# Kernel optimization log

Measured on AMD Instinct MI355X. Metric: run time of the kernel, lower is better.

## Reference

```python
import jax, jax.numpy as jnp
import numpy as np

H = 8          # n_heads
D_MODEL = 512
D_HEAD = 64    # d_keys = d_values = d_model // n_heads


def _fft_feats(x):
    # x: (B, L, C) real -> (B, C, L_fft, 3) stacking [real, imag, rfftfreq]
    n = x.shape[1]
    xf = jnp.fft.rfft(jnp.swapaxes(x, 1, 2), axis=-1)  # (B, C, L_fft) complex
    freqs = jnp.fft.rfftfreq(n).astype(x.dtype)        # (L_fft,)
    f = jnp.broadcast_to(freqs, xf.shape)
    return jnp.stack([xf.real.astype(x.dtype), xf.imag.astype(x.dtype), f], axis=-1)


def _proj_heads(feats, W, b):
    # Conv1d(kernel=3, stride=3) over the flattened (L_fft*3) axis is exactly a
    # per-frequency contraction over the 3 stacked features.
    # feats: (B, C, F, 3), W: (O, C, 3), b: (O,) -> (B, F, H, O//H)
    y = jnp.einsum('bcfk,ock->bfo', feats, W) + b
    B, F, O = y.shape
    return y.reshape(B, F, H, O // H)


def setup_inputs() -> dict:
    key = jax.random.key(0)
    ks = jax.random.split(key, 8)
    B, L, S = 16, 2048, 2048
    q = jax.random.normal(ks[0], (B, L, D_MODEL), jnp.float32)
    k = jax.random.normal(ks[1], (B, S, D_MODEL), jnp.float32)
    v = jax.random.normal(ks[2], (B, S, D_MODEL), jnp.float32)
    O = H * D_HEAD
    s = 1.0 / np.sqrt(3.0 * D_MODEL)
    Wq = jax.random.normal(ks[3], (O, D_MODEL, 3), jnp.float32) * s
    Wk = jax.random.normal(ks[4], (O, D_MODEL, 3), jnp.float32) * s
    Wv = jax.random.normal(ks[5], (O, D_MODEL, 3), jnp.float32) * s
    bq = jnp.zeros((O,), jnp.float32)
    bk = jnp.zeros((O,), jnp.float32)
    bv = jnp.zeros((O,), jnp.float32)
    Wo = jax.random.normal(ks[6], (2 * D_MODEL, O), jnp.float32) * (1.0 / np.sqrt(O))
    bo = jnp.zeros((2 * D_MODEL,), jnp.float32)
    return {"queries": q, "keys": k, "values": v,
            "Wq": Wq, "bq": bq, "Wk": Wk, "bk": bk, "Wv": Wv, "bv": bv,
            "Wo": Wo, "bo": bo}


def reference(queries, keys, values, Wq, bq, Wk, bk, Wv, bv, Wo, bo):
    B, L, _ = queries.shape
    qh = _proj_heads(_fft_feats(queries), Wq, bq)  # (B, Lf, H, E)
    kh = _proj_heads(_fft_feats(keys), Wk, bk)     # (B, Sf, H, E)
    vh = _proj_heads(_fft_feats(values), Wv, bv)   # (B, Sf, H, D)
    scale = 1.0 / jnp.sqrt(jnp.asarray(qh.shape[-1], qh.dtype))
    scores = jnp.einsum('blhe,bshe->bhls', qh, kh)
    attn = jax.nn.softmax(scale * scores, axis=-1)  # (B, H, Lf, Sf)
    ctx = jnp.einsum('bhls,bshd->blhd', attn, vh)   # (B, Lf, H, D)
    Lf = ctx.shape[1]
    ctx = ctx.reshape(B, Lf, H * D_HEAD)
    y = ctx @ Wo.T + bo                              # (B, Lf, 2*d_model)
    y = y.reshape(B, Lf, D_MODEL, 2)
    yc = jax.lax.complex(y[..., 0], y[..., 1])       # (B, Lf, d_model)
    out = jnp.fft.irfft(jnp.swapaxes(yc, 1, 2), n=L, axis=-1)  # (B, d_model, L)
    return jnp.swapaxes(out, 1, 2), attn
```

## Files before the change

### kernel.cpp

```cpp
#include <hip/hip_runtime.h>
#include <math.h>

#define FL 1025

typedef __bf16 bf16x8 __attribute__((ext_vector_type(8)));
typedef float  f32x4  __attribute__((ext_vector_type(4)));

static __device__ __forceinline__ bf16x8 ldfrag(const __bf16* p) {
  union { uint4 q; bf16x8 v; } u;
  u.q = *(const uint4*)p;
  return u.v;
}
static __device__ __forceinline__ float fexp(float x) { return __expf(x); }

static __device__ __forceinline__ void fft2048_stages(float* re, float* im, int tid, int dir) {
  for (int len = 2; len <= 2048; len <<= 1) {
    int half = len >> 1;
    __syncthreads();
    for (int t = tid; t < 1024; t += 256) {
      int j  = t & (half - 1);
      int i0 = ((t & ~(half - 1)) << 1) | j;
      int i1 = i0 + half;
      float ang = (2.0f * (float)j) / (float)len;
      float wr = cospif(ang);
      float s  = sinpif(ang);
      float wi = (dir > 0) ? s : -s;
      float vr = re[i1], vi = im[i1];
      float tr = vr * wr - vi * wi;
      float ti = vr * wi + vi * wr;
      float ur = re[i0], ui = im[i0];
      re[i0] = ur + tr; im[i0] = ui + ti;
      re[i1] = ur - tr; im[i1] = ui - ti;
    }
  }
  __syncthreads();
}

__global__ __launch_bounds__(256) void rfft3_kernel(const float* __restrict__ xT,
                                                    float* __restrict__ QF3) {
  __shared__ float re[2048];
  __shared__ float im[2048];
  int c2 = blockIdx.x, b = blockIdx.y, t = blockIdx.z, tid = threadIdx.x;
  const float* pa = xT + (((long long)t * 16 + b) * 512 + 2 * c2) * 2048;
  const float* pb = pa + 2048;
  float4 a0 = *(const float4*)(pa + tid * 8);
  float4 a1 = *(const float4*)(pa + tid * 8 + 4);
  float4 b0 = *(const float4*)(pb + tid * 8);
  float4 b1 = *(const float4*)(pb + tid * 8 + 4);
  float va[8] = {a0.x, a0.y, a0.z, a0.w, a1.x, a1.y, a1.z, a1.w};
  float vb[8] = {b0.x, b0.y, b0.z, b0.w, b1.x, b1.y, b1.z, b1.w};
#pragma unroll
  for (int j = 0; j < 8; j++) {
    int l = tid * 8 + j;
    int r = __brev((unsigned)l) >> 21;
    re[r] = va[j];
    im[r] = vb[j];
  }
  fft2048_stages(re, im, tid, -1);
  float* base = QF3 + ((long long)t * 16 + b) * 1052672;
  for (int f = tid; f <= 1024; f += 256) {
    int g = (2048 - f) & 2047;
    float fr = re[f], fi = im[f], gr = re[g], gi = im[g];
    float Xar = 0.5f * (fr + gr), Xai = 0.5f * (fi - gi);
    float Xbr = 0.5f * (fi + gi), Xbi = 0.5f * (gr - fr);
    base[(long long)(2 * c2) * 1028 + f]       = Xar;
    base[(long long)(512 + 2 * c2) * 1028 + f] = Xai;
    base[(long long)(2 * c2 + 1) * 1028 + f]   = Xbr;
    base[(long long)(513 + 2 * c2) * 1028 + f] = Xbi;
  }
}

__global__ __launch_bounds__(256) void irfft3_kernel(const float* __restrict__ ybT,
                                                     float* __restrict__ out) {
  __shared__ float Yar[FL], Yai[FL], Ybr[FL], Ybi[FL];
  __shared__ float re[2048];
  __shared__ float im[2048];
  int d2 = blockIdx.x, b = blockIdx.y, tid = threadIdx.x;
  const float* yp = ybT + ((long long)b * 1024 + 4 * d2) * 1025;
  for (int f = tid; f <= 1024; f += 256) {
    Yar[f] = yp[f];
    Yai[f] = yp[1025 + f];
    Ybr[f] = yp[2050 + f];
    Ybi[f] = yp[3075 + f];
  }
  __syncthreads();
  if (tid == 0) { Yai[0] = 0.f; Yai[1024] = 0.f; Ybi[0] = 0.f; Ybi[1024] = 0.f; }
  __syncthreads();
  for (int i = tid; i < 2048; i += 256) {
    int j = __brev((unsigned)i) >> 21;
    float rr, ii;
    if (j <= 1024) { rr = Yar[j] - Ybi[j]; ii = Yai[j] + Ybr[j]; }
    else { int f = 2048 - j; rr = Yar[f] + Ybi[f]; ii = Ybr[f] - Yai[f]; }
    re[i] = rr; im[i] = ii;
  }
  fft2048_stages(re, im, tid, +1);
  float* op = out + (long long)b * 2048 * 512 + 2 * d2;
  const float sc = 1.0f / 2048.0f;
  for (int l = tid; l < 2048; l += 256) {
    float2 v = {re[l] * sc, im[l] * sc};
    *(float2*)(op + (long long)l * 512) = v;
  }
}

__global__ __launch_bounds__(256) void transpose_x(const float* __restrict__ q,
                                                   const float* __restrict__ k,
                                                   const float* __restrict__ v,
                                                   float* __restrict__ xT) {
  __shared__ float t[32][33];
  int z = blockIdx.z;
  int ti = z >> 4, b = z & 15;
  const float* x = (ti == 0) ? q : (ti == 1) ? k : v;
  int l0 = blockIdx.x * 32, c0 = blockIdx.y * 32;
  int tx = threadIdx.x & 31, ty = threadIdx.x >> 5;
  for (int i = ty; i < 32; i += 8)
    t[i][tx] = x[((long long)b * 2048 + l0 + i) * 512 + c0 + tx];
  __syncthreads();
  float* dst = xT + ((long long)ti * 16 + b) * 512 * 2048;
  for (int i = ty; i < 32; i += 8)
    dst[((long long)(c0 + i)) * 2048 + l0 + tx] = t[tx][i];
}

__global__ __launch_bounds__(256) void setup_pack(
    const float* __restrict__ Wq, const float* __restrict__ Wk,
    const float* __restrict__ Wv, const float* __restrict__ Wo,
    const float* __restrict__ bq, const float* __restrict__ bk,
    const float* __restrict__ bv,
    __bf16* __restrict__ Wth, __bf16* __restrict__ Wtl,
    __bf16* __restrict__ Woh, float* __restrict__ wf3, float* __restrict__ bias3) {
  int bx = blockIdx.x, tid = threadIdx.x;
  if (bx < 6144) {
    int e = bx * 256 + tid;
    int t = e >> 19, local = e & 524287;
    const float* W = (t == 0) ? Wq : (t == 1) ? Wk : Wv;
    int o = local >> 10, kk = local & 1023;
    int c = kk & 511, j = kk >> 9;
    float v = W[(long long)o * 1536 + c * 3 + j];
    __bf16 h = (__bf16)v;
    Wth[e] = h;
    Wtl[e] = (__bf16)(v - (float)h);
  } else if (bx < 8192) {
    int e = (bx - 6144) * 256 + tid;
    Woh[e] = (__bf16)Wo[e];
  } else if (bx < 8198) {
    int idx = (bx - 8192) * 256 + tid;
    int t = idx / 512, o = idx & 511;
    const float* W = (t == 0) ? Wq : (t == 1) ? Wk : Wv;
    float s = 0.f;
    for (int c = 0; c < 512; c++) s += W[(long long)o * 1536 + c * 3 + 2];
    wf3[idx] = s;
  } else {
    int idx = (bx - 8198) * 256 + tid;
    int t = idx / 512, o = idx & 511;
    bias3[idx] = (t == 0) ? bq[o] : (t == 1) ? bk[o] : bv[o];
  }
}

__global__ __launch_bounds__(256) void proj_gemm(
    const float* __restrict__ QF3,
    const __bf16* __restrict__ Wth, const __bf16* __restrict__ Wtl,
    const float* __restrict__ wf3, const float* __restrict__ bias3,
    __bf16* __restrict__ qhh, __bf16* __restrict__ qhl,
    __bf16* __restrict__ khh, __bf16* __restrict__ khl,
    __bf16* __restrict__ vhT, float uscale) {
  __shared__ __bf16 As[2][128][40];
  __shared__ __bf16 Bs[2][128][40];
  int tid = threadIdx.x;
  int wid = tid >> 6, lane = tid & 63;
  int lrow = lane & 15, quad = lane >> 4;
  int m0 = blockIdx.x * 128, n0 = blockIdx.y * 128;
  int z = blockIdx.z;
  int t = z >> 4, b = z & 15;
  const float* Ab = QF3 + (long long)z * 1052672;
  const __bf16* Bbh = Wth + (long long)t * 524288;
  const __bf16* Bbl = Wtl + (long long)t * 524288;

  int wm0 = (wid & 1) * 64, wn0 = (wid >> 1) * 64;
  int floc = tid & 127;
  int kg = (tid >> 7) * 4;
  const float* Acol = Ab + min(m0 + floc, 1024);
  int srow = tid >> 1, shalf = tid & 1;

  f32x4 acc[4][4];
#pragma unroll
  for (int i = 0; i < 4; i++)
#pragma unroll
    for (int j = 0; j < 4; j++) acc[i][j] = (f32x4){0.f, 0.f, 0.f, 0.f};

  for (int k0 = 0; k0 < 1024; k0 += 32) {
#pragma unroll
    for (int it = 0; it < 4; it++) {
      int kko = kg + it * 8;
      float v0 = Acol[(long long)(k0 + kko + 0) * 1028];
      float v1 = Acol[(long long)(k0 + kko + 1) * 1028];
      float v2 = Acol[(long long)(k0 + kko + 2) * 1028];
      float v3 = Acol[(long long)(k0 + kko + 3) * 1028];
      __bf16 h0 = (__bf16)v0, h1 = (__bf16)v1, h2 = (__bf16)v2, h3 = (__bf16)v3;
      unsigned short u0, u1, u2, u3;
      __builtin_memcpy(&u0, &h0, 2); __builtin_memcpy(&u1, &h1, 2);
      __builtin_memcpy(&u2, &h2, 2); __builtin_memcpy(&u3, &h3, 2);
      uint2 hu = make_uint2((unsigned)u0 | ((unsigned)u1 << 16),
                            (unsigned)u2 | ((unsigned)u3 << 16));
      __bf16 l0 = (__bf16)(v0 - (float)h0), l1 = (__bf16)(v1 - (float)h1);
      __bf16 l2 = (__bf16)(v2 - (float)h2), l3 = (__bf16)(v3 - (float)h3);
      __builtin_memcpy(&u0, &l0, 2); __builtin_memcpy(&u1, &l1, 2);
      __builtin_memcpy(&u2, &l2, 2); __builtin_memcpy(&u3, &l3, 2);
      uint2 lu = make_uint2((unsigned)u0 | ((unsigned)u1 << 16),
                            (unsigned)u2 | ((unsigned)u3 << 16));
      *(uint2*)&As[0][floc][kko] = hu;
      *(uint2*)&As[1][floc][kko] = lu;
    }
    {
      const __bf16* s = Bbh + (long long)(n0 + srow) * 1024 + k0 + shalf * 16;
      uint4* d = (uint4*)&Bs[0][srow][shalf * 16];
      d[0] = ((const uint4*)s)[0]; d[1] = ((const uint4*)s)[1];
      s = Bbl + (long long)(n0 + srow) * 1024 + k0 + shalf * 16;
      d = (uint4*)&Bs[1][srow][shalf * 16];
      d[0] = ((const uint4*)s)[0]; d[1] = ((const uint4*)s)[1];
    }
    __syncthreads();

    bf16x8 bh[4], bl[4];
#pragma unroll
    for (int nt = 0; nt < 4; nt++) {
      int r = wn0 + nt * 16 + lrow;
      bh[nt] = ldfrag(&Bs[0][r][quad * 8]);
      bl[nt] = ldfrag(&Bs[1][r][quad * 8]);
    }
#pragma unroll
    for (int mt = 0; mt < 4; mt++) {
      int r = wm0 + mt * 16 + lrow;
      bf16x8 ah = ldfrag(&As[0][r][quad * 8]);
      bf16x8 al = ldfrag(&As[1][r][quad * 8]);
#pragma unroll
      for (int nt = 0; nt < 4; nt++) {
        acc[mt][nt] = __builtin_amdgcn_mfma_f32_16x16x32_bf16(ah, bh[nt], acc[mt][nt], 0, 0, 0);
        acc[mt][nt] = __builtin_amdgcn_mfma_f32_16x16x32_bf16(ah, bl[nt], acc[mt][nt], 0, 0, 0);
        acc[mt][nt] = __builtin_amdgcn_mfma_f32_16x16x32_bf16(al, bh[nt], acc[mt][nt], 0, 0, 0);
      }
    }
    __syncthreads();
  }

  __bf16* Ch = (t == 0) ? qhh : khh;
  __bf16* Cl = (t == 0) ? qhl : khl;
#pragma unroll
  for (int mt = 0; mt < 4; mt++) {
#pragma unroll
    for (int nt = 0; nt < 4; nt++) {
      int gn = n0 + wn0 + nt * 16 + lrow;
      float bn = bias3[t * 512 + gn];
      float vn = wf3[t * 512 + gn];
      int gmb = m0 + wm0 + mt * 16 + quad * 4;
      if (t < 2) {
#pragma unroll
        for (int r = 0; r < 4; r++) {
          int gm = gmb + r;
          if (gm < FL) {
            float val = acc[mt][nt][r] + bn + uscale * (float)gm * vn;
            long long o = ((long long)b * FL + gm) * 512 + gn;
            __bf16 h = (__bf16)val;
            Ch[o] = h;
            Cl[o] = (__bf16)(val - (float)h);
          }
        }
      } else {
        int hh = gn >> 6, dd = gn & 63;
        long long ob = ((long long)(b * 8 + hh) * 64 + dd) * 1152;
#pragma unroll
        for (int r = 0; r < 4; r++) {
          int gm = gmb + r;
          if (gm < FL) {
            float val = acc[mt][nt][r] + bn + uscale * (float)gm * vn;
            vhT[ob + gm] = (__bf16)val;
          }
        }
      }
    }
  }
}

__global__ __launch_bounds__(256) void oproj_gemm(
    const __bf16* __restrict__ ctx, const __bf16* __restrict__ Woh,
    const float* __restrict__ bo, float* __restrict__ ybT) {
  __shared__ __bf16 As[128][40];
  __shared__ __bf16 Bs[128][40];
  int tid = threadIdx.x;
  int wid = tid >> 6, lane = tid & 63;
  int lrow = lane & 15, quad = lane >> 4;
  int m0 = blockIdx.x * 128, n0 = blockIdx.y * 128;
  int z = blockIdx.z;
  const __bf16* Ab = ctx + (long long)z * 524800;
  int wm0 = (wid & 1) * 64, wn0 = (wid >> 1) * 64;
  int srow = tid >> 1, shalf = tid & 1;
  int arow = min(m0 + srow, FL - 1);

  f32x4 acc[4][4];
#pragma unroll
  for (int i = 0; i < 4; i++)
#pragma unroll
    for (int j = 0; j < 4; j++) acc[i][j] = (f32x4){0.f, 0.f, 0.f, 0.f};

  for (int k0 = 0; k0 < 512; k0 += 32) {
    {
      const __bf16* s = Ab + (long long)arow * 512 + k0 + shalf * 16;
      uint4* d = (uint4*)&As[srow][shalf * 16];
      d[0] = ((const uint4*)s)[0]; d[1] = ((const uint4*)s)[1];
      s = Woh + (long long)(n0 + srow) * 512 + k0 + shalf * 16;
      d = (uint4*)&Bs[srow][shalf * 16];
      d[0] = ((const uint4*)s)[0]; d[1] = ((const uint4*)s)[1];
    }
    __syncthreads();
    bf16x8 bh[4];
#pragma unroll
    for (int nt = 0; nt < 4; nt++) bh[nt] = ldfrag(&Bs[wn0 + nt * 16 + lrow][quad * 8]);
#pragma unroll
    for (int mt = 0; mt < 4; mt++) {
      bf16x8 ah = ldfrag(&As[wm0 + mt * 16 + lrow][quad * 8]);
#pragma unroll
      for (int nt = 0; nt < 4; nt++)
        acc[mt][nt] = __builtin_amdgcn_mfma_f32_16x16x32_bf16(ah, bh[nt], acc[mt][nt], 0, 0, 0);
    }
    __syncthreads();
  }

#pragma unroll
  for (int mt = 0; mt < 4; mt++) {
#pragma unroll
    for (int nt = 0; nt < 4; nt++) {
      int gn = n0 + wn0 + nt * 16 + lrow;
      float bn = bo[gn];
      int gmb = m0 + wm0 + mt * 16 + quad * 4;
      long long ob = (long long)z * 1049600 + (long long)gn * 1025;
#pragma unroll
      for (int r = 0; r < 4; r++) {
        int gm = gmb + r;
        if (gm < FL) ybT[ob + gm] = acc[mt][nt][r] + bn;
      }
    }
  }
}

static __device__ __forceinline__ void compute_S_tile(
    const __bf16 (*Kh)[72], const __bf16 (*Kl)[72],
    const bf16x8 (&qf)[2][2], int lrow, int quad, int n0, f32x4* sa) {
#pragma unroll
  for (int nt = 0; nt < 8; nt++) sa[nt] = (f32x4){0.f, 0.f, 0.f, 0.f};
#pragma unroll
  for (int kit = 0; kit < 2; kit++) {
#pragma unroll
    for (int nt = 0; nt < 8; nt++) {
      bf16x8 kh = ldfrag(&Kh[nt * 16 + lrow][kit * 32 + quad * 8]);
      bf16x8 kl = ldfrag(&Kl[nt * 16 + lrow][kit * 32 + quad * 8]);
      sa[nt] = __builtin_amdgcn_mfma_f32_16x16x32_bf16(qf[0][kit], kh, sa[nt], 0, 0, 0);
      sa[nt] = __builtin_amdgcn_mfma_f32_16x16x32_bf16(qf[0][kit], kl, sa[nt], 0, 0, 0);
      sa[nt] = __builtin_amdgcn_mfma_f32_16x16x32_bf16(qf[1][kit], kh, sa[nt], 0, 0, 0);
    }
  }
#pragma unroll
  for (int nt = 0; nt < 8; nt++) {
    int gn = n0 + nt * 16 + lrow;
    bool ok = gn < FL;
#pragma unroll
    for (int r = 0; r < 4; r++) sa[nt][r] = ok ? sa[nt][r] * 0.125f : -INFINITY;
  }
}

__global__ __launch_bounds__(512) void flash_kernel(
    const __bf16* __restrict__ qh_h, const __bf16* __restrict__ qh_l,
    const __bf16* __restrict__ kh_h, const __bf16* __restrict__ kh_l,
    const __bf16* __restrict__ vhT,
    float* __restrict__ attn, __bf16* __restrict__ ctxb) {
  __shared__ __align__(16) char smem[54272];
  __bf16 (*Kh)[72]  = (__bf16 (*)[72])smem;
  __bf16 (*Kl)[72]  = (__bf16 (*)[72])(smem + 18432);
  __bf16 (*P)[136]  = (__bf16 (*)[136])smem;
  __bf16 (*Bv)[136] = (__bf16 (*)[136])(smem + 36864);

  int tid = threadIdx.x;
  int wid = tid >> 6, lane = tid & 63;
  int lrow = lane & 15, quad = lane >> 4;
  int f0 = blockIdx.x * 128;
  int z = blockIdx.z;
  int b = z >> 3, h = z & 7;

  bf16x8 qf[2][2];
  {
    int rowq = min(f0 + wid * 16 + lrow, FL - 1);
    long long base = ((long long)b * FL + rowq) * 512 + h * 64 + quad * 8;
#pragma unroll
    for (int kit = 0; kit < 2; kit++) {
      qf[0][kit] = ldfrag(qh_h + base + kit * 32);
      qf[1][kit] = ldfrag(qh_l + base + kit * 32);
    }
  }

  int sp = tid >> 8, srw = (tid >> 1) & 127, shalf = tid & 1;
  const __bf16* ksrc0 = (sp ? kh_l : kh_h) + (long long)b * FL * 512 + h * 64 + shalf * 32;
  __bf16* kdst = (sp ? Kl[srw] : Kh[srw]) + shalf * 32;

  float m_i[4], l_i[4];
#pragma unroll
  for (int r = 0; r < 4; r++) { m_i[r] = -INFINITY; l_i[r] = 0.f; }

  f32x4 sa[8];

  for (int nt0 = 0; nt0 < 9; nt0++) {
    __syncthreads();
    {
      int srowg = min(nt0 * 128 + srw, FL - 1);
      const __bf16* s = ksrc0 + (long long)srowg * 512;
#pragma unroll
      for (int u = 0; u < 4; u++) ((uint4*)kdst)[u] = ((const uint4*)s)[u];
    }
    __syncthreads();
    compute_S_tile(Kh, Kl, qf, lrow, quad, nt0 * 128, sa);
#pragma unroll
    for (int r = 0; r < 4; r++) {
      float mx = -INFINITY;
#pragma unroll
      for (int nt = 0; nt < 8; nt++) mx = fmaxf(mx, sa[nt][r]);
      for (int o = 1; o < 16; o <<= 1) mx = fmaxf(mx, __shfl_xor(mx, o, 64));
      float mn = fmaxf(m_i[r], mx);
      float al = fexp(m_i[r] - mn);
      float ps = 0.f;
#pragma unroll
      for (int nt = 0; nt < 8; nt++) ps += fexp(sa[nt][r] - mn);
      for (int o = 1; o < 16; o <<= 1) ps += __shfl_xor(ps, o, 64);
      l_i[r] = l_i[r] * al + ps;
      m_i[r] = mn;
    }
  }

  float rl[4];
#pragma unroll
  for (int r = 0; r < 4; r++) rl[r] = 1.0f / l_i[r];

  f32x4 oa[4];
#pragma unroll
  for (int j = 0; j < 4; j++) oa[j] = (f32x4){0.f, 0.f, 0.f, 0.f};

  int vrow = tid >> 3, voff = (tid & 7) * 16;
  const __bf16* vsrc0 = vhT + ((long long)z * 64 + vrow) * 1152 + voff;
  __bf16* vdst = &Bv[vrow][voff];

  float* attnz = attn + (long long)z * 1050625;
  for (int nt0 = 0; nt0 < 9; nt0++) {
    __syncthreads();
    {
      int srowg = min(nt0 * 128 + srw, FL - 1);
      const __bf16* s = ksrc0 + (long long)srowg * 512;
#pragma unroll
      for (int u = 0; u < 4; u++) ((uint4*)kdst)[u] = ((const uint4*)s)[u];
      const __bf16* vs = vsrc0 + nt0 * 128;
      ((uint4*)vdst)[0] = ((const uint4*)vs)[0];
      ((uint4*)vdst)[1] = ((const uint4*)vs)[1];
    }
    __syncthreads();
    compute_S_tile(Kh, Kl, qf, lrow, quad, nt0 * 128, sa);
    __syncthreads();
#pragma unroll
    for (int nt = 0; nt < 8; nt++) {
      int gn = nt0 * 128 + nt * 16 + lrow;
#pragma unroll
      for (int r = 0; r < 4; r++) {
        float p = fexp(sa[nt][r] - m_i[r]) * rl[r];
        int lm = wid * 16 + quad * 4 + r;
        int gm = f0 + lm;
        if (gm < FL && gn < FL) attnz[(long long)gm * FL + gn] = p;
        P[lm][nt * 16 + lrow] = (__bf16)p;
      }
    }
#pragma unroll
    for (int kk = 0; kk < 4; kk++) {
      bf16x8 pf = ldfrag(&P[wid * 16 + lrow][kk * 32 + quad * 8]);
#pragma unroll
      for (int nto = 0; nto < 4; nto++) {
        bf16x8 vf = ldfrag(&Bv[nto * 16 + lrow][kk * 32 + quad * 8]);
        oa[nto] = __builtin_amdgcn_mfma_f32_16x16x32_bf16(pf, vf, oa[nto], 0, 0, 0);
      }
    }
  }

#pragma unroll
  for (int nto = 0; nto < 4; nto++) {
#pragma unroll
    for (int r = 0; r < 4; r++) {
      int gm = f0 + wid * 16 + quad * 4 + r;
      if (gm < FL)
        ctxb[((long long)b * FL + gm) * 512 + h * 64 + nto * 16 + lrow] = (__bf16)oa[nto][r];
    }
  }
}

extern "C" void kernel_launch(void* const* d_in, const int* in_sizes, int n_in,
                              void* d_out, int out_size, void* d_ws, size_t ws_size,
                              hipStream_t stream) {
  (void)in_sizes; (void)n_in; (void)out_size; (void)ws_size;
  const float* q  = (const float*)d_in[0];
  const float* k  = (const float*)d_in[1];
  const float* v  = (const float*)d_in[2];
  const float* Wq = (const float*)d_in[3];
  const float* bq = (const float*)d_in[4];
  const float* Wk = (const float*)d_in[5];
  const float* bk = (const float*)d_in[6];
  const float* Wv = (const float*)d_in[7];
  const float* bv = (const float*)d_in[8];
  const float* Wo = (const float*)d_in[9];
  const float* bo = (const float*)d_in[10];

  float* outp = (float*)d_out;
  float* attn = outp + (long long)16 * 2048 * 512;

  float* ws = (float*)d_ws;
  float*  xT   = ws;
  float*  QF3  = xT + 50331648;
  float*  wf3  = QF3 + 50528256;
  float*  bias3= wf3 + 1536;
  __bf16* Wth  = (__bf16*)(bias3 + 1536);
  __bf16* Wtl  = Wth + 1572864;
  __bf16* Woh  = Wtl + 1572864;
  __bf16* qhh  = Woh + 524288;
  __bf16* qhl  = qhh + 8396800;
  __bf16* khh  = qhl + 8396800;
  __bf16* khl  = khh + 8396800;
  __bf16* vhT  = khl + 8396800;
  __bf16* ctx  = (__bf16*)QF3;
  float*  ybT  = xT;

  transpose_x<<<dim3(64, 16, 48), 256, 0, stream>>>(q, k, v, xT);
  setup_pack<<<dim3(8204, 1, 1), 256, 0, stream>>>(Wq, Wk, Wv, Wo, bq, bk, bv,
                                                   Wth, Wtl, Woh, wf3, bias3);
  rfft3_kernel<<<dim3(256, 16, 3), 256, 0, stream>>>(xT, QF3);

  proj_gemm<<<dim3(9, 4, 48), 256, 0, stream>>>(
      QF3, Wth, Wtl, wf3, bias3, qhh, qhl, khh, khl, vhT, 1.0f / 2048.0f);

  flash_kernel<<<dim3(9, 1, 128), 512, 0, stream>>>(
      qhh, qhl, khh, khl, vhT, attn, ctx);

  oproj_gemm<<<dim3(9, 8, 16), 256, 0, stream>>>(ctx, Woh, bo, ybT);

  irfft3_kernel<<<dim3(256, 16), 256, 0, stream>>>(ybT, outp);
}
```

Measured before the change: 1.793 ms.

## Pre-split FFT outputs into bf16 hi/lo pairs and remap blocks across XCDs

The rFFT kernel now stores each spectral value as a packed bf16 hi/lo pair instead of fp32, so proj_gemm only does bit shuffles instead of per-element splitting. It is meant to remove the conversion ALU work from the GEMM's A-tile load path. Several kernels (proj_gemm, oproj_gemm, flash, irfft) also remap their linear block index so that consecutive blocks sharing operands land on the same XCD (stride-8 interleave), aiming for better L2 reuse on the MI355X's chiplet layout. The remap assumes grid sizes divisible by 8, and it changes the order in which blocks run.

Measured after the change: 1.680 ms. 1.07x faster.

```diff
diff --git a/kernel.cpp b/kernel.cpp
--- a/kernel.cpp
+++ b/kernel.cpp
@@ -12,6 +12,16 @@
   return u.v;
 }
 static __device__ __forceinline__ float fexp(float x) { return __expf(x); }
+
+static __device__ __forceinline__ unsigned pack_hl(float v) {
+  __bf16 h = (__bf16)v;
+  float hf = (float)h;
+  __bf16 l = (__bf16)(v - hf);
+  unsigned short uh, ul;
+  __builtin_memcpy(&uh, &h, 2);
+  __builtin_memcpy(&ul, &l, 2);
+  return (unsigned)uh | ((unsigned)ul << 16);
+}
 
 static __device__ __forceinline__ void fft2048_stages(float* re, float* im, int tid, int dir) {
   for (int len = 2; len <= 2048; len <<= 1) {
@@ -37,7 +47,7 @@
 }
 
 __global__ __launch_bounds__(256) void rfft3_kernel(const float* __restrict__ xT,
-                                                    float* __restrict__ QF3) {
+                                                    unsigned* __restrict__ QF3) {
   __shared__ float re[2048];
   __shared__ float im[2048];
   int c2 = blockIdx.x, b = blockIdx.y, t = blockIdx.z, tid = threadIdx.x;
@@ -57,16 +67,16 @@
     im[r] = vb[j];
   }
   fft2048_stages(re, im, tid, -1);
-  float* base = QF3 + ((long long)t * 16 + b) * 1052672;
+  unsigned* base = QF3 + ((long long)t * 16 + b) * 1052672;
   for (int f = tid; f <= 1024; f += 256) {
     int g = (2048 - f) & 2047;
     float fr = re[f], fi = im[f], gr = re[g], gi = im[g];
     float Xar = 0.5f * (fr + gr), Xai = 0.5f * (fi - gi);
     float Xbr = 0.5f * (fi + gi), Xbi = 0.5f * (gr - fr);
-    base[(long long)(2 * c2) * 1028 + f]       = Xar;
-    base[(long long)(512 + 2 * c2) * 1028 + f] = Xai;
-    base[(long long)(2 * c2 + 1) * 1028 + f]   = Xbr;
-    base[(long long)(513 + 2 * c2) * 1028 + f] = Xbi;
+    base[(long long)(2 * c2) * 1028 + f]       = pack_hl(Xar);
+    base[(long long)(512 + 2 * c2) * 1028 + f] = pack_hl(Xai);
+    base[(long long)(2 * c2 + 1) * 1028 + f]   = pack_hl(Xbr);
+    base[(long long)(513 + 2 * c2) * 1028 + f] = pack_hl(Xbi);
   }
 }
 
@@ -75,7 +85,11 @@
   __shared__ float Yar[FL], Yai[FL], Ybr[FL], Ybi[FL];
   __shared__ float re[2048];
   __shared__ float im[2048];
-  int d2 = blockIdx.x, b = blockIdx.y, tid = threadIdx.x;
+  int lin = blockIdx.y * 256 + blockIdx.x;
+  int w = (lin & 7) * 512 + (lin >> 3);
+  int d2 = w & 255;
+  int b = w >> 8;
+  int tid = threadIdx.x;
   const float* yp = ybT + ((long long)b * 1024 + 4 * d2) * 1025;
   for (int f = tid; f <= 1024; f += 256) {
     Yar[f] = yp[f];
@@ -156,7 +170,7 @@
 }
 
 __global__ __launch_bounds__(256) void proj_gemm(
-    const float* __restrict__ QF3,
+    const unsigned* __restrict__ QF3,
     const __bf16* __restrict__ Wth, const __bf16* __restrict__ Wtl,
     const float* __restrict__ wf3, const float* __restrict__ bias3,
     __bf16* __restrict__ qhh, __bf16* __restrict__ qhl,
@@ -167,17 +181,21 @@
   int tid = threadIdx.x;
   int wid = tid >> 6, lane = tid & 63;
   int lrow = lane & 15, quad = lane >> 4;
-  int m0 = blockIdx.x * 128, n0 = blockIdx.y * 128;
-  int z = blockIdx.z;
+  int lin = (blockIdx.z * 4 + blockIdx.y) * 9 + blockIdx.x;
+  int w = (lin & 7) * 216 + (lin >> 3);
+  int m0 = (w % 9) * 128;
+  int rem = w / 9;
+  int n0 = (rem & 3) * 128;
+  int z = rem >> 2;
   int t = z >> 4, b = z & 15;
-  const float* Ab = QF3 + (long long)z * 1052672;
+  const unsigned* Ab = QF3 + (long long)z * 1052672;
   const __bf16* Bbh = Wth + (long long)t * 524288;
   const __bf16* Bbl = Wtl + (long long)t * 524288;
 
   int wm0 = (wid & 1) * 64, wn0 = (wid >> 1) * 64;
   int floc = tid & 127;
   int kg = (tid >> 7) * 4;
-  const float* Acol = Ab + min(m0 + floc, 1024);
+  const unsigned* Acol = Ab + min(m0 + floc, 1024);
   int srow = tid >> 1, shalf = tid & 1;
 
   f32x4 acc[4][4];
@@ -190,22 +208,14 @@
 #pragma unroll
     for (int it = 0; it < 4; it++) {
       int kko = kg + it * 8;
-      float v0 = Acol[(long long)(k0 + kko + 0) * 1028];
-      float v1 = Acol[(long long)(k0 + kko + 1) * 1028];
-      float v2 = Acol[(long long)(k0 + kko + 2) * 1028];
-      float v3 = Acol[(long long)(k0 + kko + 3) * 1028];
-      __bf16 h0 = (__bf16)v0, h1 = (__bf16)v1, h2 = (__bf16)v2, h3 = (__bf16)v3;
-      unsigned short u0, u1, u2, u3;
-      __builtin_memcpy(&u0, &h0, 2); __builtin_memcpy(&u1, &h1, 2);
-      __builtin_memcpy(&u2, &h2, 2); __builtin_memcpy(&u3, &h3, 2);
-      uint2 hu = make_uint2((unsigned)u0 | ((unsigned)u1 << 16),
-                            (unsigned)u2 | ((unsigned)u3 << 16));
-      __bf16 l0 = (__bf16)(v0 - (float)h0), l1 = (__bf16)(v1 - (float)h1);
-      __bf16 l2 = (__bf16)(v2 - (float)h2), l3 = (__bf16)(v3 - (float)h3);
-      __builtin_memcpy(&u0, &l0, 2); __builtin_memcpy(&u1, &l1, 2);
-      __builtin_memcpy(&u2, &l2, 2); __builtin_memcpy(&u3, &l3, 2);
-      uint2 lu = make_uint2((unsigned)u0 | ((unsigned)u1 << 16),
-                            (unsigned)u2 | ((unsigned)u3 << 16));
+      unsigned u0 = Acol[(long long)(k0 + kko + 0) * 1028];
+      unsigned u1 = Acol[(long long)(k0 + kko + 1) * 1028];
+      unsigned u2 = Acol[(long long)(k0 + kko + 2) * 1028];
+      unsigned u3 = Acol[(long long)(k0 + kko + 3) * 1028];
+      uint2 hu = make_uint2((u0 & 0xffffu) | (u1 << 16),
+                            (u2 & 0xffffu) | (u3 << 16));
+      uint2 lu = make_uint2((u0 >> 16) | (u1 & 0xffff0000u),
+                            (u2 >> 16) | (u3 & 0xffff0000u));
       *(uint2*)&As[0][floc][kko] = hu;
       *(uint2*)&As[1][floc][kko] = lu;
     }
@@ -287,8 +297,12 @@
   int tid = threadIdx.x;
   int wid = tid >> 6, lane = tid & 63;
   int lrow = lane & 15, quad = lane >> 4;
-  int m0 = blockIdx.x * 128, n0 = blockIdx.y * 128;
-  int z = blockIdx.z;
+  int lin = (blockIdx.z * 8 + blockIdx.y) * 9 + blockIdx.x;
+  int w = (lin & 7) * 144 + (lin >> 3);
+  int m0 = (w % 9) * 128;
+  int rem = w / 9;
+  int n0 = (rem & 7) * 128;
+  int z = rem >> 3;
   const __bf16* Ab = ctx + (long long)z * 524800;
   int wm0 = (wid & 1) * 64, wn0 = (wid >> 1) * 64;
   int srow = tid >> 1, shalf = tid & 1;
@@ -379,8 +393,10 @@
   int tid = threadIdx.x;
   int wid = tid >> 6, lane = tid & 63;
   int lrow = lane & 15, quad = lane >> 4;
-  int f0 = blockIdx.x * 128;
-  int z = blockIdx.z;
+  int lin = blockIdx.z * 9 + blockIdx.x;
+  int w = (lin & 7) * 144 + (lin >> 3);
+  int f0 = (w % 9) * 128;
+  int z = w / 9;
   int b = z >> 3, h = z & 7;
 
   bf16x8 qf[2][2];
@@ -530,10 +546,11 @@
   transpose_x<<<dim3(64, 16, 48), 256, 0, stream>>>(q, k, v, xT);
   setup_pack<<<dim3(8204, 1, 1), 256, 0, stream>>>(Wq, Wk, Wv, Wo, bq, bk, bv,
                                                    Wth, Wtl, Woh, wf3, bias3);
-  rfft3_kernel<<<dim3(256, 16, 3), 256, 0, stream>>>(xT, QF3);
+  rfft3_kernel<<<dim3(256, 16, 3), 256, 0, stream>>>(xT, (unsigned*)QF3);
 
   proj_gemm<<<dim3(9, 4, 48), 256, 0, stream>>>(
-      QF3, Wth, Wtl, wf3, bias3, qhh, qhl, khh, khl, vhT, 1.0f / 2048.0f);
+      (const unsigned*)QF3, Wth, Wtl, wf3, bias3, qhh, qhl, khh, khl, vhT,
+      1.0f / 2048.0f);
 
   flash_kernel<<<dim3(9, 1, 128), 512, 0, stream>>>(
       qhh, qhl, khh, khl, vhT, attn, ctx);
```
